# Optimization experiments

Hardware: AMD Instinct MI355X
Metric: run time of the kernel (lower is better)

Reference implementation:

```python
import jax, jax.numpy as jnp
import numpy as np

D_MODEL = 1024
N_HEADS = 16
HEAD_DIM = D_MODEL // N_HEADS


def setup_inputs() -> dict:
    key = jax.random.key(0)
    ks = jax.random.split(key, 6)
    s = 1.0 / np.sqrt(D_MODEL)
    x = jax.random.normal(ks[0], (4, 2048, D_MODEL), dtype=jnp.float32)
    Wq = jax.random.uniform(ks[1], (D_MODEL, D_MODEL), jnp.float32, -s, s)
    Wk = jax.random.uniform(ks[2], (D_MODEL, D_MODEL), jnp.float32, -s, s)
    Wv = jax.random.uniform(ks[3], (D_MODEL, D_MODEL), jnp.float32, -s, s)
    Wo = jax.random.uniform(ks[4], (D_MODEL, D_MODEL), jnp.float32, -s, s)
    bo = jax.random.uniform(ks[5], (D_MODEL,), jnp.float32, -s, s)
    return {"x": x, "Wq": Wq, "Wk": Wk, "Wv": Wv, "Wo": Wo, "bo": bo}


def reference(x, Wq, Wk, Wv, Wo, bo):
    B, S, _ = x.shape
    # nn.Linear: x @ W.T
    def proj(W):
        return (x @ W.T).reshape(B, S, N_HEADS, HEAD_DIM).transpose(0, 2, 1, 3)
    q = proj(Wq)  # [B,H,S,Dh]
    k = proj(Wk)
    v = proj(Wv)
    scores = jnp.einsum("bhqd,bhkd->bhqk", q, k) / jnp.sqrt(jnp.float32(HEAD_DIM))
    attn = jax.nn.softmax(scores, axis=-1)
    out = jnp.einsum("bhqk,bhkd->bhqd", attn, v)
    out = out.transpose(0, 2, 1, 3).reshape(B, S, D_MODEL)
    return out @ Wo.T + bo
```

## Files before the change

### kernel.cpp

```cpp
#include <hip/hip_runtime.h>
#include <hip/hip_bf16.h>
#include <math.h>

#define BB 4
#define SS 2048
#define DM 1024
#define NH 16
#define DH 64
#define MROWS (BB*SS)

typedef __attribute__((ext_vector_type(8))) short bf16x8;
typedef __attribute__((ext_vector_type(4))) float f32x4;
typedef __attribute__((ext_vector_type(8))) unsigned short u16x8;

__device__ __forceinline__ unsigned short f2b(float f) {
    __hip_bfloat16 b = __float2bfloat16(f);
    return *reinterpret_cast<unsigned short*>(&b);
}

__device__ __forceinline__ void gload_lds16(const void* g, void* l) {
    __builtin_amdgcn_global_load_lds((const __attribute__((address_space(1))) unsigned int*)g,
                                     (__attribute__((address_space(3))) unsigned int*)l,
                                     16, 0, 0);
}

__global__ __launch_bounds__(256) void cast_x_kernel(const float* __restrict__ in,
                                                     unsigned short* __restrict__ out) {
    const size_t i = ((size_t)blockIdx.x * 256 + threadIdx.x) * 8;
    const float4 a = *(const float4*)(in + i);
    const float4 b = *(const float4*)(in + i + 4);
    unsigned short pk[8] = {f2b(a.x), f2b(a.y), f2b(a.z), f2b(a.w),
                            f2b(b.x), f2b(b.y), f2b(b.z), f2b(b.w)};
    *(u16x8*)(out + i) = *(u16x8*)pk;
}

__global__ __launch_bounds__(256) void cast_w_kernel(const float* __restrict__ Wq,
                                                     const float* __restrict__ Wk,
                                                     const float* __restrict__ Wv,
                                                     const float* __restrict__ Wo,
                                                     unsigned short* __restrict__ out) {
    const float* src = (blockIdx.y == 0) ? Wq : (blockIdx.y == 1) ? Wk
                     : (blockIdx.y == 2) ? Wv : Wo;
    const size_t i = ((size_t)blockIdx.x * 256 + threadIdx.x) * 8;
    const float4 a = *(const float4*)(src + i);
    const float4 b = *(const float4*)(src + i + 4);
    unsigned short pk[8] = {f2b(a.x), f2b(a.y), f2b(a.z), f2b(a.w),
                            f2b(b.x), f2b(b.y), f2b(b.z), f2b(b.w)};
    *(u16x8*)(out + (size_t)blockIdx.y * DM * DM + i) = *(u16x8*)pk;
}

template<int MODE>
__global__ __launch_bounds__(256) void gemm_mfma(const unsigned short* __restrict__ A,
                                                 const unsigned short* __restrict__ Wq,
                                                 const unsigned short* __restrict__ Wk,
                                                 const unsigned short* __restrict__ Wv,
                                                 unsigned short* __restrict__ Oq,
                                                 unsigned short* __restrict__ Ok,
                                                 unsigned short* __restrict__ Ov,
                                                 float* __restrict__ outf,
                                                 const float* __restrict__ bias) {
    __shared__ unsigned short As[128 * 64];
    __shared__ unsigned short Bs[128 * 64];
    const int t  = threadIdx.x;
    const int l  = t & 63;
    const int w  = t >> 6;
    const int g  = l >> 4;
    const int cc = l & 15;
    const int wr = w >> 1, wc = w & 1;
    const int m0 = blockIdx.x * 128;
    const int n0 = blockIdx.y * 128;

    const unsigned short* W;
    unsigned short* Ob = nullptr;
    float oscale = 1.f;
    if (MODE == 0) {
        const int z = blockIdx.z;
        W  = (z == 0) ? Wq : (z == 1) ? Wk : Wv;
        Ob = (z == 0) ? Oq : (z == 1) ? Ok : Ov;
        if (z == 0) oscale = 0.125f;
    } else {
        W = Wq;
    }

    const f32x4 zf = {0.f, 0.f, 0.f, 0.f};
    f32x4 acc[4][4] = {{zf,zf,zf,zf},{zf,zf,zf,zf},{zf,zf,zf,zf},{zf,zf,zf,zf}};

    for (int k0 = 0; k0 < DM; k0 += 64) {
        __syncthreads();
        #pragma unroll
        for (int i = 0; i < 4; ++i) {
            const int s   = i * 256 + t;
            const int row = s >> 3;
            const int j   = s & 7;
            const int gb  = j ^ (row & 7);
            gload_lds16(A + (size_t)(m0 + row) * DM + k0 + gb * 8, &As[s * 8]);
            gload_lds16(W + (size_t)(n0 + row) * DM + k0 + gb * 8, &Bs[s * 8]);
        }
        asm volatile("s_waitcnt vmcnt(0)" ::: "memory");
        __syncthreads();

        #pragma unroll
        for (int kk = 0; kk < 2; ++kk) {
            bf16x8 af[4], bf[4];
            #pragma unroll
            for (int mi = 0; mi < 4; ++mi) {
                const int row = wr * 64 + mi * 16 + cc;
                const int jb  = (kk * 4 + g) ^ (row & 7);
                af[mi] = *(const bf16x8*)&As[(row * 8 + jb) * 8];
            }
            #pragma unroll
            for (int ni = 0; ni < 4; ++ni) {
                const int row = wc * 64 + ni * 16 + cc;
                const int jb  = (kk * 4 + g) ^ (row & 7);
                bf[ni] = *(const bf16x8*)&Bs[(row * 8 + jb) * 8];
            }
            #pragma unroll
            for (int mi = 0; mi < 4; ++mi)
                #pragma unroll
                for (int ni = 0; ni < 4; ++ni)
                    acc[mi][ni] = __builtin_amdgcn_mfma_f32_16x16x32_bf16(af[mi], bf[ni], acc[mi][ni], 0, 0, 0);
        }
    }

    #pragma unroll
    for (int mi = 0; mi < 4; ++mi) {
        #pragma unroll
        for (int r = 0; r < 4; ++r) {
            const int m = m0 + wr * 64 + mi * 16 + 4 * g + r;
            if (MODE == 0) {
                const int b = m >> 11, s = m & 2047;
                #pragma unroll
                for (int ni = 0; ni < 4; ++ni) {
                    const int col = n0 + wc * 64 + ni * 16 + cc;
                    const int h = col >> 6, dh = col & 63;
                    Ob[((size_t)(b * NH + h) * SS + s) * DH + dh] = f2b(acc[mi][ni][r] * oscale);
                }
            } else {
                #pragma unroll
                for (int ni = 0; ni < 4; ++ni) {
                    const int col = n0 + wc * 64 + ni * 16 + cc;
                    outf[(size_t)m * DM + col] = acc[mi][ni][r] + bias[col];
                }
            }
        }
    }
}

__global__ __launch_bounds__(256) void transpose_v(const unsigned short* __restrict__ Vb,
                                                   unsigned short* __restrict__ Vt) {
    __shared__ unsigned short T[64][72];
    const int t  = threadIdx.x;
    const int bh = blockIdx.y;
    const int s0 = blockIdx.x * 64;
    #pragma unroll
    for (int r = 0; r < 2; ++r) {
        const int idx = t + 256 * r;
        const int row = idx >> 3;
        const int d8  = (idx & 7) * 8;
        *(u16x8*)&T[row][d8] = *(const u16x8*)(Vb + ((size_t)bh * SS + s0 + row) * 64 + d8);
    }
    __syncthreads();
    const int d  = t >> 2;
    const int sc = (t & 3) * 16;
    unsigned short tmp[16];
    #pragma unroll
    for (int i = 0; i < 16; ++i) tmp[i] = T[sc + i][d];
    unsigned short* dst = Vt + ((size_t)bh * 64 + d) * SS + s0 + sc;
    *(u16x8*)(dst)     = *(u16x8*)&tmp[0];
    *(u16x8*)(dst + 8) = *(u16x8*)&tmp[8];
}

__global__ __launch_bounds__(256) void attn_mfma(const unsigned short* __restrict__ Qb,
                                                 const unsigned short* __restrict__ Kb,
                                                 const unsigned short* __restrict__ Vtp,
                                                 unsigned short* __restrict__ AOb) {
    __shared__ unsigned short Ks[64*64];
    __shared__ unsigned short Vs[64*64];
    __shared__ unsigned short Ps[64*64];
    const int t    = threadIdx.x;
    const int lane = t & 63;
    const int w    = t >> 6;
    const int g    = lane >> 4;
    const int cc   = lane & 15;
    const int bh   = blockIdx.y;
    const int q0   = blockIdx.x * 64;

    const unsigned short* Qw = Qb + ((size_t)bh * SS + q0 + w * 16 + cc) * 64;
    const bf16x8 qf0 = *(const bf16x8*)(Qw + 8 * g);
    const bf16x8 qf1 = *(const bf16x8*)(Qw + 32 + 8 * g);

    const unsigned short* Kbase = Kb  + (size_t)bh * SS * 64;
    const unsigned short* Vbase = Vtp + (size_t)bh * 64 * SS;

    const f32x4 zf = {0.f, 0.f, 0.f, 0.f};
    f32x4 oacc[4] = {zf, zf, zf, zf};
    float mrow[4] = {-INFINITY, -INFINITY, -INFINITY, -INFINITY};
    float lrow[4] = {0.f, 0.f, 0.f, 0.f};

    for (int kt = 0; kt < SS / 64; ++kt) {
        __syncthreads();
        #pragma unroll
        for (int r2 = 0; r2 < 2; ++r2) {
            const int idx = t + 256 * r2;
            const int row = idx >> 3;
            const int g8  = idx & 7;
            *(u16x8*)&Ks[row * 64 + ((g8 ^ (row & 7)) << 3)] =
                *(const u16x8*)(Kbase + ((size_t)(kt * 64 + row)) * 64 + g8 * 8);
            *(u16x8*)&Vs[row * 64 + ((g8 ^ (row & 7)) << 3)] =
                *(const u16x8*)(Vbase + (size_t)row * SS + kt * 64 + g8 * 8);
        }
        __syncthreads();

        f32x4 sacc[4] = {zf, zf, zf, zf};
        #pragma unroll
        for (int n = 0; n < 4; ++n) {
            const int key = n * 16 + cc;
            const bf16x8 kf0 = *(const bf16x8*)&Ks[key * 64 + ((g       ^ (key & 7)) << 3)];
            const bf16x8 kf1 = *(const bf16x8*)&Ks[key * 64 + (((4 + g) ^ (key & 7)) << 3)];
            sacc[n] = __builtin_amdgcn_mfma_f32_16x16x32_bf16(qf0, kf0, sacc[n], 0, 0, 0);
            sacc[n] = __builtin_amdgcn_mfma_f32_16x16x32_bf16(qf1, kf1, sacc[n], 0, 0, 0);
        }

        float p[4][4];
        float scl[4];
        #pragma unroll
        for (int r = 0; r < 4; ++r) {
            float mx = fmaxf(fmaxf(sacc[0][r], sacc[1][r]), fmaxf(sacc[2][r], sacc[3][r]));
            mx = fmaxf(mx, __shfl_xor(mx, 1));
            mx = fmaxf(mx, __shfl_xor(mx, 2));
            mx = fmaxf(mx, __shfl_xor(mx, 4));
            mx = fmaxf(mx, __shfl_xor(mx, 8));
            const float nm = fmaxf(mrow[r], mx);
            scl[r] = __expf(mrow[r] - nm);
            mrow[r] = nm;
            float rs = 0.f;
            #pragma unroll
            for (int n = 0; n < 4; ++n) {
                const float pv = __expf(sacc[n][r] - nm);
                p[n][r] = pv;
                rs += pv;
            }
            rs += __shfl_xor(rs, 1);
            rs += __shfl_xor(rs, 2);
            rs += __shfl_xor(rs, 4);
            rs += __shfl_xor(rs, 8);
            lrow[r] = lrow[r] * scl[r] + rs;
        }

        #pragma unroll
        for (int n = 0; n < 4; ++n)
            #pragma unroll
            for (int r = 0; r < 4; ++r) {
                const int qr  = w * 16 + g * 4 + r;
                const int key = n * 16 + cc;
                Ps[qr * 64 + (key ^ ((qr & 7) << 3))] = f2b(p[n][r]);
            }

        #pragma unroll
        for (int n = 0; n < 4; ++n) {
            oacc[n][0] *= scl[0]; oacc[n][1] *= scl[1];
            oacc[n][2] *= scl[2]; oacc[n][3] *= scl[3];
        }

        const int qrow = w * 16 + cc;
        #pragma unroll
        for (int ks = 0; ks < 2; ++ks) {
            const bf16x8 pf = *(const bf16x8*)&Ps[qrow * 64 + (((ks * 4 + g) ^ (qrow & 7)) << 3)];
            #pragma unroll
            for (int n = 0; n < 4; ++n) {
                const int vrow = n * 16 + cc;
                const bf16x8 vf = *(const bf16x8*)&Vs[vrow * 64 + (((ks * 4 + g) ^ (vrow & 7)) << 3)];
                oacc[n] = __builtin_amdgcn_mfma_f32_16x16x32_bf16(pf, vf, oacc[n], 0, 0, 0);
            }
        }
    }

    const int b = bh >> 4, h = bh & 15;
    #pragma unroll
    for (int r = 0; r < 4; ++r) {
        const float inv  = 1.f / lrow[r];
        const int   srow = q0 + w * 16 + g * 4 + r;
        unsigned short* dst = AOb + ((size_t)(b * SS + srow)) * DM + h * 64;
        dst[ 0 + cc] = f2b(oacc[0][r] * inv);
        dst[16 + cc] = f2b(oacc[1][r] * inv);
        dst[32 + cc] = f2b(oacc[2][r] * inv);
        dst[48 + cc] = f2b(oacc[3][r] * inv);
    }
}

extern "C" void kernel_launch(void* const* d_in, const int* in_sizes, int n_in,
                              void* d_out, int out_size, void* d_ws, size_t ws_size,
                              hipStream_t stream) {
    const float* x  = (const float*)d_in[0];
    const float* Wq = (const float*)d_in[1];
    const float* Wk = (const float*)d_in[2];
    const float* Wv = (const float*)d_in[3];
    const float* Wo = (const float*)d_in[4];
    const float* bo = (const float*)d_in[5];
    float* out = (float*)d_out;

    const size_t NEL = (size_t)MROWS * DM;
    unsigned short* xb  = (unsigned short*)d_ws;
    unsigned short* Wb  = xb + NEL;
    unsigned short* Qb  = Wb + (size_t)4 * DM * DM;
    unsigned short* Kb  = Qb + NEL;
    unsigned short* Vb  = Kb + NEL;
    unsigned short* Vt  = Vb + NEL;
    unsigned short* AOb = Vt + NEL;

    const dim3 blk(256);
    cast_x_kernel<<<dim3(NEL / (256 * 8)), blk, 0, stream>>>(x, xb);
    cast_w_kernel<<<dim3(DM * DM / (256 * 8), 4), blk, 0, stream>>>(Wq, Wk, Wv, Wo, Wb);

    gemm_mfma<0><<<dim3(MROWS / 128, DM / 128, 3), blk, 0, stream>>>(
        xb, Wb, Wb + (size_t)DM * DM, Wb + (size_t)2 * DM * DM,
        Qb, Kb, Vb, nullptr, nullptr);

    transpose_v<<<dim3(SS / 64, BB * NH), blk, 0, stream>>>(Vb, Vt);
    attn_mfma<<<dim3(SS / 64, BB * NH), blk, 0, stream>>>(Qb, Kb, Vt, AOb);

    gemm_mfma<1><<<dim3(MROWS / 128, DM / 128, 1), blk, 0, stream>>>(
        AOb, Wb + (size_t)3 * DM * DM, nullptr, nullptr,
        nullptr, nullptr, nullptr, out, bo);
}
```

Before: 397.6 us.

## Double-buffer attention K/V tiles via async LDS loads and use exp2 softmax

The attention kernel now stages K and V tiles into two LDS buffers with global_load_lds, prefetching the next tile while the current one is computed, and uses vmcnt waits in place of the synchronous load-then-barrier pattern. The softmax scale folds log2(e) into the Q projection scale so raw v_exp_f32 (exp2) can replace __expf. s_setprio is raised around the MFMA sections. This trades extra LDS footprint, which may lower occupancy, for hiding global-load latency and fewer ALU ops per exponential.

```diff
diff --git a/kernel.cpp b/kernel.cpp
--- a/kernel.cpp
+++ b/kernel.cpp
@@ -8,6 +8,7 @@
 #define NH 16
 #define DH 64
 #define MROWS (BB*SS)
+#define NT (SS/64)
 
 typedef __attribute__((ext_vector_type(8))) short bf16x8;
 typedef __attribute__((ext_vector_type(4))) float f32x4;
@@ -16,6 +17,12 @@
 __device__ __forceinline__ unsigned short f2b(float f) {
     __hip_bfloat16 b = __float2bfloat16(f);
     return *reinterpret_cast<unsigned short*>(&b);
+}
+
+__device__ __forceinline__ float fexp2(float x) {
+    float r;
+    asm("v_exp_f32 %0, %1" : "=v"(r) : "v"(x));
+    return r;
 }
 
 __device__ __forceinline__ void gload_lds16(const void* g, void* l) {
@@ -59,8 +66,8 @@
                                                  unsigned short* __restrict__ Ov,
                                                  float* __restrict__ outf,
                                                  const float* __restrict__ bias) {
-    __shared__ unsigned short As[128 * 64];
-    __shared__ unsigned short Bs[128 * 64];
+    __shared__ __align__(16) unsigned short As[128 * 64];
+    __shared__ __align__(16) unsigned short Bs[128 * 64];
     const int t  = threadIdx.x;
     const int l  = t & 63;
     const int w  = t >> 6;
@@ -77,7 +84,7 @@
         const int z = blockIdx.z;
         W  = (z == 0) ? Wq : (z == 1) ? Wk : Wv;
         Ob = (z == 0) ? Oq : (z == 1) ? Ok : Ov;
-        if (z == 0) oscale = 0.125f;
+        if (z == 0) oscale = 0.18033688011112042f;
     } else {
         W = Wq;
     }
@@ -174,8 +181,8 @@
                                                  const unsigned short* __restrict__ Kb,
                                                  const unsigned short* __restrict__ Vtp,
                                                  unsigned short* __restrict__ AOb) {
-    __shared__ unsigned short Ks[64*64];
-    __shared__ unsigned short Vs[64*64];
+    __shared__ __align__(16) unsigned short Ks[2][64*64];
+    __shared__ __align__(16) unsigned short Vs[2][64*64];
     __shared__ unsigned short Ps[64*64];
     const int t    = threadIdx.x;
     const int lane = t & 63;
@@ -192,34 +199,46 @@
     const unsigned short* Kbase = Kb  + (size_t)bh * SS * 64;
     const unsigned short* Vbase = Vtp + (size_t)bh * 64 * SS;
 
+    auto stage = [&](int buf, int kt) {
+        #pragma unroll
+        for (int r2 = 0; r2 < 2; ++r2) {
+            const int idx = r2 * 256 + t;
+            const int row = idx >> 3;
+            const int gb  = (idx & 7) ^ (row & 7);
+            gload_lds16(Kbase + (size_t)(kt * 64 + row) * 64 + gb * 8, &Ks[buf][idx * 8]);
+            gload_lds16(Vbase + (size_t)row * SS + kt * 64 + gb * 8, &Vs[buf][idx * 8]);
+        }
+    };
+
+    asm volatile("s_waitcnt vmcnt(0)" ::: "memory");
+    stage(0, 0);
+
     const f32x4 zf = {0.f, 0.f, 0.f, 0.f};
     f32x4 oacc[4] = {zf, zf, zf, zf};
     float mrow[4] = {-INFINITY, -INFINITY, -INFINITY, -INFINITY};
     float lrow[4] = {0.f, 0.f, 0.f, 0.f};
 
-    for (int kt = 0; kt < SS / 64; ++kt) {
+    for (int kt = 0; kt < NT; ++kt) {
+        const int cur = kt & 1;
+        if (kt + 1 < NT) {
+            stage(cur ^ 1, kt + 1);
+            asm volatile("s_waitcnt vmcnt(4)" ::: "memory");
+        } else {
+            asm volatile("s_waitcnt vmcnt(0)" ::: "memory");
+        }
         __syncthreads();
-        #pragma unroll
-        for (int r2 = 0; r2 < 2; ++r2) {
-            const int idx = t + 256 * r2;
-            const int row = idx >> 3;
-            const int g8  = idx & 7;
-            *(u16x8*)&Ks[row * 64 + ((g8 ^ (row & 7)) << 3)] =
-                *(const u16x8*)(Kbase + ((size_t)(kt * 64 + row)) * 64 + g8 * 8);
-            *(u16x8*)&Vs[row * 64 + ((g8 ^ (row & 7)) << 3)] =
-                *(const u16x8*)(Vbase + (size_t)row * SS + kt * 64 + g8 * 8);
-        }
-        __syncthreads();
 
         f32x4 sacc[4] = {zf, zf, zf, zf};
+        __builtin_amdgcn_s_setprio(1);
         #pragma unroll
         for (int n = 0; n < 4; ++n) {
             const int key = n * 16 + cc;
-            const bf16x8 kf0 = *(const bf16x8*)&Ks[key * 64 + ((g       ^ (key & 7)) << 3)];
-            const bf16x8 kf1 = *(const bf16x8*)&Ks[key * 64 + (((4 + g) ^ (key & 7)) << 3)];
+            const bf16x8 kf0 = *(const bf16x8*)&Ks[cur][key * 64 + ((g       ^ (key & 7)) << 3)];
+            const bf16x8 kf1 = *(const bf16x8*)&Ks[cur][key * 64 + (((4 + g) ^ (key & 7)) << 3)];
             sacc[n] = __builtin_amdgcn_mfma_f32_16x16x32_bf16(qf0, kf0, sacc[n], 0, 0, 0);
             sacc[n] = __builtin_amdgcn_mfma_f32_16x16x32_bf16(qf1, kf1, sacc[n], 0, 0, 0);
         }
+        __builtin_amdgcn_s_setprio(0);
 
         float p[4][4];
         float scl[4];
@@ -231,12 +250,12 @@
             mx = fmaxf(mx, __shfl_xor(mx, 4));
             mx = fmaxf(mx, __shfl_xor(mx, 8));
             const float nm = fmaxf(mrow[r], mx);
-            scl[r] = __expf(mrow[r] - nm);
+            scl[r] = fexp2(mrow[r] - nm);
             mrow[r] = nm;
             float rs = 0.f;
             #pragma unroll
             for (int n = 0; n < 4; ++n) {
-                const float pv = __expf(sacc[n][r] - nm);
+                const float pv = fexp2(sacc[n][r] - nm);
                 p[n][r] = pv;
                 rs += pv;
             }
@@ -263,16 +282,20 @@
         }
 
         const int qrow = w * 16 + cc;
+        __builtin_amdgcn_s_setprio(1);
         #pragma unroll
         for (int ks = 0; ks < 2; ++ks) {
             const bf16x8 pf = *(const bf16x8*)&Ps[qrow * 64 + (((ks * 4 + g) ^ (qrow & 7)) << 3)];
             #pragma unroll
             for (int n = 0; n < 4; ++n) {
                 const int vrow = n * 16 + cc;
-                const bf16x8 vf = *(const bf16x8*)&Vs[vrow * 64 + (((ks * 4 + g) ^ (vrow & 7)) << 3)];
+                const bf16x8 vf = *(const bf16x8*)&Vs[cur][vrow * 64 + (((ks * 4 + g) ^ (vrow & 7)) << 3)];
                 oacc[n] = __builtin_amdgcn_mfma_f32_16x16x32_bf16(pf, vf, oacc[n], 0, 0, 0);
             }
         }
+        __builtin_amdgcn_s_setprio(0);
+
+        __syncthreads();
     }
 
     const int b = bh >> 4, h = bh & 15;
```

Measured after the change: 384.4 us. -3.3%, faster.
